# Performance work log

Hardware: AMD Instinct MI355X
Metric: run time of the kernel (lower is better)

## Reference

```python
import jax, jax.numpy as jnp
import numpy as np

N_NODES = 100000
N_EDGES = 3200000
NUM_TYPES = 8
TYPE_DIM = 16
IN_DIM = 5
HID = 64
HEADS = 2
OUT = 64
LN_EPS = 1e-5
NEG_SLOPE = 0.2


def segment_softmax(logits, seg, num_segments):
    # logits: [E, H], seg: [E] destination ids
    m = jax.ops.segment_max(logits, seg, num_segments=num_segments)
    m = jnp.where(jnp.isfinite(m), m, 0.0)
    e = jnp.exp(logits - m[seg])
    s = jax.ops.segment_sum(e, seg, num_segments=num_segments)
    return e / (s[seg] + 1e-16)


def gat_conv(x, W, a_src, a_dst, b, src, dst, n_nodes, heads, ch):
    # x: [N, F_in], W: [F_in, heads*ch], a_src/a_dst: [heads, ch], b: [heads*ch]
    h = (x @ W).reshape(n_nodes, heads, ch)            # [N, H, C]
    al_s = jnp.einsum('nhc,hc->nh', h, a_src)          # [N, H]
    al_d = jnp.einsum('nhc,hc->nh', h, a_dst)          # [N, H]
    e = jax.nn.leaky_relu(al_s[src] + al_d[dst], NEG_SLOPE)  # [E, H]
    alpha = segment_softmax(e, dst, n_nodes)           # [E, H]
    msg = alpha[:, :, None] * h[src]                   # [E, H, C]
    out = jax.ops.segment_sum(msg, dst, num_segments=n_nodes)  # [N, H, C]
    return out.reshape(n_nodes, heads * ch) + b


def setup_inputs() -> dict:
    key = jax.random.key(0)
    ks = jax.random.split(key, 16)
    in1 = IN_DIM + TYPE_DIM  # 21
    inp = {
        'x': jax.random.normal(ks[0], (N_NODES, IN_DIM), dtype=jnp.float32),
        'edge_index': jax.random.randint(ks[1], (2, N_EDGES), 0, N_NODES, dtype=jnp.int32),
        'type_ids': jax.random.randint(ks[2], (N_NODES,), 0, NUM_TYPES, dtype=jnp.int32),
        'type_emb': jax.random.normal(ks[3], (NUM_TYPES, TYPE_DIM), dtype=jnp.float32) * 0.3,
        'W1': jax.random.normal(ks[4], (in1, HID), dtype=jnp.float32) * (1.0 / np.sqrt(in1)),
        'a_src1': jax.random.normal(ks[5], (HEADS, HID // HEADS), dtype=jnp.float32) * 0.1,
        'a_dst1': jax.random.normal(ks[6], (HEADS, HID // HEADS), dtype=jnp.float32) * 0.1,
        'b1': jnp.zeros((HID,), dtype=jnp.float32),
        'W2': jax.random.normal(ks[7], (HID, OUT), dtype=jnp.float32) * (1.0 / np.sqrt(HID)),
        'a_src2': jax.random.normal(ks[8], (1, OUT), dtype=jnp.float32) * 0.1,
        'a_dst2': jax.random.normal(ks[9], (1, OUT), dtype=jnp.float32) * 0.1,
        'b2': jnp.zeros((OUT,), dtype=jnp.float32),
        'gamma': jnp.ones((OUT,), dtype=jnp.float32),
        'beta': jnp.zeros((OUT,), dtype=jnp.float32),
    }
    return inp


def reference(x, type_emb, W1, a_src1, a_dst1, b1, W2, a_src2, a_dst2, b2, gamma, beta, edge_index, type_ids):
    n = x.shape[0]
    # type embedding concat
    xin = jnp.concatenate([x, type_emb[type_ids]], axis=1)  # [N, 21]
    # add self loops (PyG GATConv default)
    loops = jnp.arange(n, dtype=edge_index.dtype)
    src = jnp.concatenate([edge_index[0], loops])
    dst = jnp.concatenate([edge_index[1], loops])
    h = gat_conv(xin, W1, a_src1, a_dst1, b1, src, dst, n, HEADS, HID // HEADS)
    h = jax.nn.relu(h)  # dropout = identity at inference
    h = gat_conv(h, W2, a_src2, a_dst2, b2, src, dst, n, 1, OUT)
    # LayerNorm
    mu = jnp.mean(h, axis=-1, keepdims=True)
    var = jnp.var(h, axis=-1, keepdims=True)
    return (h - mu) / jnp.sqrt(var + LN_EPS) * gamma + beta
```

## Files before the change

kernel.cpp:

```cpp
#include <hip/hip_runtime.h>
#include <hip/hip_fp16.h>

#define NEG_SLOPE 0.2f
#define BKT_SHIFT 8
#define BKT_NODES 256
#define BKT_CAP 10240
#define SRC_SHIFT 18
#define SRC_MASK 0x3FFFF
#define CHUNK 8192
#define NBMAX 512

typedef _Float16 half8 __attribute__((ext_vector_type(8)));
typedef float float4v __attribute__((ext_vector_type(4)));

__global__ void k_node1(const float* __restrict__ x, const int* __restrict__ type_ids,
                        const float* __restrict__ type_emb, const float* __restrict__ W1,
                        const float* __restrict__ a_src1, const float* __restrict__ a_dst1,
                        __half2* __restrict__ h1h, float* __restrict__ als1, float* __restrict__ ald1,
                        int N)
{
    int node = blockIdx.x * 4 + (threadIdx.x >> 6);
    int j = threadIdx.x & 63;
    if (node >= N) return;

    float xin[21];
#pragma unroll
    for (int k = 0; k < 5; k++) xin[k] = x[node * 5 + k];
    int t = type_ids[node];
#pragma unroll
    for (int k = 0; k < 16; k++) xin[5 + k] = type_emb[t * 16 + k];

    float h = 0.f;
#pragma unroll
    for (int k = 0; k < 21; k++) h += xin[k] * W1[k * 64 + j];

    float hn = __shfl_xor(h, 1);
    if ((j & 1) == 0)
        h1h[node * 32 + (j >> 1)] = __floats2half2_rn(h, hn);

    int head = j >> 5, lane = j & 31;
    float ps = h * a_src1[head * 32 + lane];
    float pd = h * a_dst1[head * 32 + lane];
#pragma unroll
    for (int m = 16; m >= 1; m >>= 1) { ps += __shfl_xor(ps, m); pd += __shfl_xor(pd, m); }
    if (lane == 0) { als1[node * 2 + head] = ps; ald1[node * 2 + head] = pd; }
}

__global__ __launch_bounds__(512) void k_bucketA(
        const int* __restrict__ ei, unsigned int* __restrict__ pk,
        int* __restrict__ bcnt, int E, int NBKT)
{
    __shared__ unsigned int stage[CHUNK];
    __shared__ unsigned short stageB[CHUNK];
    __shared__ int cnt[NBMAX];
    __shared__ int excl[NBMAX];
    __shared__ int curp[NBMAX];
    __shared__ int gbase[NBMAX];

    int t = threadIdx.x;
    int e0 = blockIdx.x * CHUNK;
    bool vec4 = ((E & 3) == 0);

    cnt[t] = 0;
    __syncthreads();

    int4 s4[4], d4[4];
    bool val[4];

    if (vec4) {
#pragma unroll
        for (int it = 0; it < 4; it++) {
            int e = e0 + it * 2048 + t * 4;
            val[it] = (e < E);
            if (val[it]) {
                s4[it] = *(const int4*)(ei + e);
                d4[it] = *(const int4*)(ei + (size_t)E + e);
                atomicAdd(&cnt[d4[it].x >> BKT_SHIFT], 1);
                atomicAdd(&cnt[d4[it].y >> BKT_SHIFT], 1);
                atomicAdd(&cnt[d4[it].z >> BKT_SHIFT], 1);
                atomicAdd(&cnt[d4[it].w >> BKT_SHIFT], 1);
            }
        }
    } else {
        for (int i = t; i < CHUNK; i += 512) {
            int e = e0 + i;
            if (e >= E) break;
            atomicAdd(&cnt[ei[E + e] >> BKT_SHIFT], 1);
        }
    }
    __syncthreads();
    int myc = cnt[t];
    __syncthreads();
    for (int off = 1; off < NBMAX; off <<= 1) {
        int v = (t >= off) ? cnt[t - off] : 0;
        __syncthreads();
        cnt[t] += v;
        __syncthreads();
    }
    {
        int ex = cnt[t] - myc;
        excl[t] = ex;
        curp[t] = ex;
        if (t < NBKT)
            gbase[t] = (myc > 0) ? atomicAdd(&bcnt[t], myc) : 0;
    }
    __syncthreads();
    if (vec4) {
#pragma unroll
        for (int it = 0; it < 4; it++) {
            if (!val[it]) continue;
            int ss[4] = {s4[it].x, s4[it].y, s4[it].z, s4[it].w};
            int dd[4] = {d4[it].x, d4[it].y, d4[it].z, d4[it].w};
#pragma unroll
            for (int k = 0; k < 4; k++) {
                int b = dd[k] >> BKT_SHIFT;
                int p = atomicAdd(&curp[b], 1);
                stage[p] = (unsigned)ss[k] | ((unsigned)(dd[k] & (BKT_NODES - 1)) << SRC_SHIFT);
                stageB[p] = (unsigned short)b;
            }
        }
    } else {
        for (int i = t; i < CHUNK; i += 512) {
            int e = e0 + i;
            if (e >= E) break;
            int s = ei[e], d = ei[E + e];
            int b = d >> BKT_SHIFT;
            int p = atomicAdd(&curp[b], 1);
            stage[p] = (unsigned)s | ((unsigned)(d & (BKT_NODES - 1)) << SRC_SHIFT);
            stageB[p] = (unsigned short)b;
        }
    }
    __syncthreads();
    int total = E - e0; if (total > CHUNK) total = CHUNK;
    for (int i = t; i < total; i += 512) {
        int b = stageB[i];
        int idx = gbase[b] + (i - excl[b]);
        if (idx < BKT_CAP) pk[(size_t)b * BKT_CAP + idx] = stage[i];
    }
}

__global__ __launch_bounds__(512) void k_build(
        const unsigned int* __restrict__ pk, const int* __restrict__ bcnt,
        int* __restrict__ rs, int* __restrict__ cur,
        int* __restrict__ ssrc, int N)
{
    __shared__ unsigned int vals[BKT_CAP];
    __shared__ int cnt[BKT_NODES];
    __shared__ int cursor[BKT_NODES];
    __shared__ int orig[BKT_NODES];
    __shared__ int red[512];
    int b = blockIdx.x;
    int t = threadIdx.x;
    int nb = min(bcnt[b], BKT_CAP);

    int part = 0;
    for (int i = t; i < b; i += 512) part += min(bcnt[i], BKT_CAP);
    red[t] = part;
    if (t < BKT_NODES) cnt[t] = 0;
    __syncthreads();
    for (int off = 256; off; off >>= 1) {
        if (t < off) red[t] += red[t + off];
        __syncthreads();
    }
    int bs = red[0];

    const unsigned int* mypk = pk + (size_t)b * BKT_CAP;
    int nb4 = nb & ~3;
    for (int e = t * 4; e < nb4; e += 2048) {
        uint4 v = *(const uint4*)(mypk + e);
        *(uint4*)(vals + e) = v;
        atomicAdd(&cnt[v.x >> SRC_SHIFT], 1);
        atomicAdd(&cnt[v.y >> SRC_SHIFT], 1);
        atomicAdd(&cnt[v.z >> SRC_SHIFT], 1);
        atomicAdd(&cnt[v.w >> SRC_SHIFT], 1);
    }
    for (int e = nb4 + t; e < nb; e += 512) {
        unsigned int v = mypk[e];
        vals[e] = v;
        atomicAdd(&cnt[v >> SRC_SHIFT], 1);
    }
    __syncthreads();
    if (t < BKT_NODES) orig[t] = cnt[t];
    __syncthreads();
    for (int off = 1; off < BKT_NODES; off <<= 1) {
        int v = (t < BKT_NODES && t >= off) ? cnt[t - off] : 0;
        __syncthreads();
        if (t < BKT_NODES) cnt[t] += v;
        __syncthreads();
    }
    if (t < BKT_NODES) {
        int c = orig[t];
        int ex = cnt[t] - c;
        cursor[t] = ex;
        int node = (b << BKT_SHIFT) + t;
        if (node < N) { rs[node] = bs + ex; cur[node] = bs + ex + c; }
    }
    __syncthreads();
    for (int e = t; e < nb; e += 512) {
        unsigned int w = vals[e];
        int p = atomicAdd(&cursor[w >> SRC_SHIFT], 1);
        ssrc[bs + p] = (int)(w & SRC_MASK);
    }
}

__global__ void k_gather1(const int* __restrict__ rs, const int* __restrict__ cur,
                          const int* __restrict__ ssrc, const float4* __restrict__ h4,
                          const float* __restrict__ als1, const float* __restrict__ ald1,
                          const float* __restrict__ b1, float4* __restrict__ h2h4, int N)
{
    int t = threadIdx.x;
    int l = t & 63;
    int q = l & 15;
    int i = q & 7;
    int hlf = q >> 3;
    int grpbase = l & 48;
    int head = i >> 2;

    int node = blockIdx.x * 16 + (t >> 4);
    bool live = node < N;
    int node_c = live ? node : (N - 1);

    int beg = rs[node_c];
    int cnt = live ? (cur[node_c] - beg) : 0;

    float ad0 = ald1[node_c * 2 + 0];
    float ad1 = ald1[node_c * 2 + 1];
    float ad = head ? ad1 : ad0;

    int mc = cnt;
    mc = max(mc, __shfl_xor(mc, 16));
    mc = max(mc, __shfl_xor(mc, 32));

    float acc[8];
#pragma unroll
    for (int k = 0; k < 8; k++) acc[k] = 0.f;
    float wsum = 0.f;

    for (int b = 0; b < mc; b += 16) {
        int slot = b + q;
        bool valid = slot < cnt;
        int idx = valid ? (beg + slot) : 0;
        int s = ssrc[idx];
        if (!valid) s = node_c;
        float2 al = *(const float2*)(als1 + (size_t)s * 2);
        float lg0 = al.x + ad0; lg0 = (lg0 >= 0.f) ? lg0 : NEG_SLOPE * lg0;
        float lg1 = al.y + ad1; lg1 = (lg1 >= 0.f) ? lg1 : NEG_SLOPE * lg1;
        float w0 = valid ? __expf(lg0) : 0.f;
        float w1 = valid ? __expf(lg1) : 0.f;
        __half2 wp = __floats2half2_rn(w0, w1);
        unsigned wpi = *(unsigned*)&wp;

#pragma unroll
        for (int r = 0; r < 8; r++) {
            int srcl = grpbase + hlf * 8 + r;
            int sr = __shfl(s, srcl);
            unsigned wri = __shfl(wpi, srcl);
            __half2 wh = *(__half2*)&wri;
            float w = head ? __high2float(wh) : __low2float(wh);
            float4 rv = h4[(size_t)sr * 8 + i];
            const __half* hp = (const __half*)&rv;
#pragma unroll
            for (int k = 0; k < 8; k++)
                acc[k] = fmaf(w, __half2float(hp[k]), acc[k]);
            wsum += w;
        }
    }

#pragma unroll
    for (int k = 0; k < 8; k++) acc[k] += __shfl_xor(acc[k], 8);
    wsum += __shfl_xor(wsum, 8);

    {
        float lg = als1[node_c * 2 + head] + ad;
        lg = (lg >= 0.f) ? lg : NEG_SLOPE * lg;
        float w = __expf(lg);
        float4 rv = h4[(size_t)node_c * 8 + i];
        const __half* hp = (const __half*)&rv;
#pragma unroll
        for (int k = 0; k < 8; k++)
            acc[k] = fmaf(w, __half2float(hp[k]), acc[k]);
        wsum += w;
    }

    float inv = 1.f / (wsum + 1e-16f);
    if (live && hlf == 0) {
        union { float4 f4; __half2 h2[4]; } u;
#pragma unroll
        for (int c = 0; c < 4; c++) {
            float v0 = fmaxf(acc[2*c]   * inv + b1[i * 8 + 2*c],     0.f);
            float v1 = fmaxf(acc[2*c+1] * inv + b1[i * 8 + 2*c + 1], 0.f);
            u.h2[c] = __floats2half2_rn(v0, v1);
        }
        h2h4[(size_t)node * 8 + i] = u.f4;
    }
}

__global__ __launch_bounds__(256) void k_node2m(
        const _Float16* __restrict__ h2h, const float* __restrict__ W2,
        const float* __restrict__ a_src2, const float* __restrict__ a_dst2,
        _Float16* __restrict__ h3h, float* __restrict__ als2, float* __restrict__ ald2, int N)
{
    __shared__ _Float16 w2t[64][72];
    __shared__ float h3t[4][16][65];
    int t = threadIdx.x;
    for (int e = t; e < 4096; e += 256) {
        int k = e >> 6, n = e & 63;
        w2t[n][k] = (_Float16)W2[e];
    }
    __syncthreads();

    int w = t >> 6, l = t & 63;
    int l15 = l & 15, quad = l >> 4;
    int nodebase = blockIdx.x * 64 + w * 16;

    int arow = nodebase + l15;
    if (arow >= N) arow = N - 1;
    const half8* ap = (const half8*)(h2h + (size_t)arow * 64 + quad * 8);
    half8 a0 = ap[0];
    half8 a1 = ap[4];
    float4v accs[4];
#pragma unroll
    for (int nt = 0; nt < 4; nt++) {
        half8 b0 = *(const half8*)(&w2t[nt * 16 + l15][quad * 8]);
        half8 b1 = *(const half8*)(&w2t[nt * 16 + l15][32 + quad * 8]);
        float4v c = {0.f, 0.f, 0.f, 0.f};
        c = __builtin_amdgcn_mfma_f32_16x16x32_f16(a0, b0, c, 0, 0, 0);
        c = __builtin_amdgcn_mfma_f32_16x16x32_f16(a1, b1, c, 0, 0, 0);
        accs[nt] = c;
    }
#pragma unroll
    for (int nt = 0; nt < 4; nt++)
#pragma unroll
        for (int r = 0; r < 4; r++)
            h3t[w][quad * 4 + r][nt * 16 + l15] = accs[nt][r];
    __syncthreads();

    int m = l >> 2, part = l & 3;
    int g = blockIdx.x * 64 + w * 16 + m;
    float ps = 0.f, pd = 0.f;
    union { float4 f4[2]; _Float16 h[16]; } u;
#pragma unroll
    for (int c = 0; c < 16; c++) {
        float v = h3t[w][m][part * 16 + c];
        ps += v * a_src2[part * 16 + c];
        pd += v * a_dst2[part * 16 + c];
        u.h[c] = (_Float16)v;
    }
    if (g < N) {
        float4* dst = (float4*)(h3h + (size_t)g * 64) + part * 2;
        dst[0] = u.f4[0];
        dst[1] = u.f4[1];
    }
    ps += __shfl_xor(ps, 1); ps += __shfl_xor(ps, 2);
    pd += __shfl_xor(pd, 1); pd += __shfl_xor(pd, 2);
    if (part == 0 && g < N) { als2[g] = ps; ald2[g] = pd; }
}

__global__ void k_gather2(const int* __restrict__ rs, const int* __restrict__ cur,
                          const int* __restrict__ ssrc, const float4* __restrict__ h4,
                          const float* __restrict__ als2, const float* __restrict__ ald2,
                          const float* __restrict__ b2, const float* __restrict__ gamma,
                          const float* __restrict__ beta, float* __restrict__ out, int N)
{
    int t = threadIdx.x;
    int l = t & 63;
    int q = l & 15;
    int i = q & 7;
    int hlf = q >> 3;
    int grpbase = l & 48;

    int node = blockIdx.x * 16 + (t >> 4);
    bool live = node < N;
    int node_c = live ? node : (N - 1);

    int beg = rs[node_c];
    int cnt = live ? (cur[node_c] - beg) : 0;
    float ad = ald2[node_c];

    int mc = cnt;
    mc = max(mc, __shfl_xor(mc, 16));
    mc = max(mc, __shfl_xor(mc, 32));

    float acc[8];
#pragma unroll
    for (int k = 0; k < 8; k++) acc[k] = 0.f;
    float wsum = 0.f;

    for (int b = 0; b < mc; b += 16) {
        int slot = b + q;
        bool valid = slot < cnt;
        int idx = valid ? (beg + slot) : 0;
        int s = ssrc[idx];
        if (!valid) s = node_c;
        float lg = als2[s] + ad;
        lg = (lg >= 0.f) ? lg : NEG_SLOPE * lg;
        float w = valid ? __expf(lg) : 0.f;

#pragma unroll
        for (int r = 0; r < 8; r++) {
            int srcl = grpbase + hlf * 8 + r;
            int sr = __shfl(s, srcl);
            float wr = __shfl(w, srcl);
            float4 rv = h4[(size_t)sr * 8 + i];
            const __half* hp = (const __half*)&rv;
#pragma unroll
            for (int k = 0; k < 8; k++)
                acc[k] = fmaf(wr, __half2float(hp[k]), acc[k]);
            wsum += wr;
        }
    }

#pragma unroll
    for (int k = 0; k < 8; k++) acc[k] += __shfl_xor(acc[k], 8);
    wsum += __shfl_xor(wsum, 8);

    {
        float lg = als2[node_c] + ad;
        lg = (lg >= 0.f) ? lg : NEG_SLOPE * lg;
        float w = __expf(lg);
        float4 rv = h4[(size_t)node_c * 8 + i];
        const __half* hp = (const __half*)&rv;
#pragma unroll
        for (int k = 0; k < 8; k++)
            acc[k] = fmaf(w, __half2float(hp[k]), acc[k]);
        wsum += w;
    }

    float inv = 1.f / (wsum + 1e-16f);
    float o[8];
    float s = 0.f;
#pragma unroll
    for (int k = 0; k < 8; k++) { o[k] = acc[k] * inv + b2[i * 8 + k]; s += o[k]; }
    s += __shfl_xor(s, 1); s += __shfl_xor(s, 2); s += __shfl_xor(s, 4);
    float mu = s * (1.f / 64.f);
    float v = 0.f;
#pragma unroll
    for (int k = 0; k < 8; k++) { float d = o[k] - mu; v += d * d; }
    v += __shfl_xor(v, 1); v += __shfl_xor(v, 2); v += __shfl_xor(v, 4);
    v *= (1.f / 64.f);
    float rstd = rsqrtf(v + 1e-5f);
    if (live && hlf == 0) {
        float res[8];
#pragma unroll
        for (int k = 0; k < 8; k++)
            res[k] = (o[k] - mu) * rstd * gamma[i * 8 + k] + beta[i * 8 + k];
        float4* op = (float4*)(out + (size_t)node * 64 + i * 8);
        op[0] = make_float4(res[0], res[1], res[2], res[3]);
        op[1] = make_float4(res[4], res[5], res[6], res[7]);
    }
}

extern "C" void kernel_launch(void* const* d_in, const int* in_sizes, int n_in,
                              void* d_out, int out_size, void* d_ws, size_t ws_size,
                              hipStream_t stream) {
    const float* x        = (const float*)d_in[0];
    const int*   ei       = (const int*)  d_in[1];
    const int*   type_ids = (const int*)  d_in[2];
    const float* type_emb = (const float*)d_in[3];
    const float* W1       = (const float*)d_in[4];
    const float* a_src1   = (const float*)d_in[5];
    const float* a_dst1   = (const float*)d_in[6];
    const float* b1       = (const float*)d_in[7];
    const float* W2       = (const float*)d_in[8];
    const float* a_src2   = (const float*)d_in[9];
    const float* a_dst2   = (const float*)d_in[10];
    const float* b2       = (const float*)d_in[11];
    const float* gamma    = (const float*)d_in[12];
    const float* beta     = (const float*)d_in[13];

    int N = in_sizes[0] / 5;
    int E = in_sizes[1] / 2;
    int NBKT = (N + BKT_NODES - 1) >> BKT_SHIFT;

    char* base = (char*)d_ws;
    size_t off = 0;
    auto carve = [&](size_t bytes) { void* p = base + off; off += (bytes + 255) & ~(size_t)255; return p; };
    __half2* h1h = (__half2*)carve((size_t)N * 64 * sizeof(__half));
    size_t pk_bytes = (size_t)NBKT * BKT_CAP * sizeof(unsigned int);
    size_t h23_bytes = 2 * (size_t)N * 64 * sizeof(__half);
    char* uni = (char*)carve(pk_bytes > h23_bytes ? pk_bytes : h23_bytes);
    _Float16* h2h = (_Float16*)uni;
    _Float16* h3h = (_Float16*)(uni + (size_t)N * 64 * sizeof(__half));
    unsigned int* pk = (unsigned int*)uni;
    float* als1  = (float*)carve((size_t)N * 2 * sizeof(float));
    float* ald1  = (float*)carve((size_t)N * 2 * sizeof(float));
    float* als2  = (float*)carve((size_t)N * sizeof(float));
    float* ald2  = (float*)carve((size_t)N * sizeof(float));
    int*   rs    = (int*)carve((size_t)N * sizeof(int));
    int*   cur   = (int*)carve((size_t)N * sizeof(int));
    int*   bcnt  = (int*)carve(1024 * sizeof(int));
    int*   ssrc  = (int*)carve((size_t)E * sizeof(int) + 256);

    dim3 tb(256);
    dim3 tb512(512);

    k_node1<<<dim3((N + 3) / 4), tb, 0, stream>>>(x, type_ids, type_emb, W1, a_src1, a_dst1,
                                                  h1h, als1, ald1, N);

    hipMemsetAsync(bcnt, 0, NBKT * sizeof(int), stream);
    k_bucketA<<<dim3((E + CHUNK - 1) / CHUNK), tb512, 0, stream>>>(ei, pk, bcnt, E, NBKT);
    k_build<<<dim3(NBKT), tb512, 0, stream>>>(pk, bcnt, rs, cur, ssrc, N);

    dim3 ng((N + 15) / 16);
    k_gather1<<<ng, tb, 0, stream>>>(rs, cur, ssrc, (const float4*)h1h, als1, ald1, b1,
                                     (float4*)h2h, N);
    k_node2m<<<dim3((N + 63) / 64), tb, 0, stream>>>(h2h, W2, a_src2, a_dst2,
                                                     h3h, als2, ald2, N);
    k_gather2<<<ng, tb, 0, stream>>>(rs, cur, ssrc, (const float4*)h3h, als2, ald2, b2,
                                     gamma, beta, (float*)d_out, N);
}
```

Measured before the change: 310.5 us.

## Use wave-shuffle scans and precompute bucket bases in separate kernel

Replaces the barrier-heavy Hillis-Steele shared-memory scans in the bucketing and CSR-build kernels with wavefront shuffle scans plus a small per-wave partial combine. A new single-block kernel computes the bucket base offsets once, so each build block no longer re-reduces all preceding bucket counts. The build kernel also drops its 40KB LDS staging of packed edges and re-reads them from global memory (likely L2), which should raise occupancy at the cost of a second global read. The extra kernel launch adds a small fixed overhead.

```diff
diff --git a/kernel.cpp b/kernel.cpp
--- a/kernel.cpp
+++ b/kernel.cpp
@@ -13,6 +13,15 @@
 typedef _Float16 half8 __attribute__((ext_vector_type(8)));
 typedef float float4v __attribute__((ext_vector_type(4)));
 
+__device__ __forceinline__ int wave_iscan(int v, int lane) {
+#pragma unroll
+    for (int off = 1; off < 64; off <<= 1) {
+        int u = __shfl_up(v, off);
+        if (lane >= off) v += u;
+    }
+    return v;
+}
+
 __global__ void k_node1(const float* __restrict__ x, const int* __restrict__ type_ids,
                         const float* __restrict__ type_emb, const float* __restrict__ W1,
                         const float* __restrict__ a_src1, const float* __restrict__ a_dst1,
@@ -56,8 +65,10 @@
     __shared__ int excl[NBMAX];
     __shared__ int curp[NBMAX];
     __shared__ int gbase[NBMAX];
+    __shared__ int wpart[8];
 
     int t = threadIdx.x;
+    int lane = t & 63, wv = t >> 6;
     int e0 = blockIdx.x * CHUNK;
     bool vec4 = ((E & 3) == 0);
 
@@ -90,15 +101,14 @@
     }
     __syncthreads();
     int myc = cnt[t];
-    __syncthreads();
-    for (int off = 1; off < NBMAX; off <<= 1) {
-        int v = (t >= off) ? cnt[t - off] : 0;
-        __syncthreads();
-        cnt[t] += v;
-        __syncthreads();
-    }
+    int incl = wave_iscan(myc, lane);
+    if (lane == 63) wpart[wv] = incl;
+    __syncthreads();
+#pragma unroll
+    for (int k = 0; k < 8; k++)
+        if (k < wv) incl += wpart[k];
     {
-        int ex = cnt[t] - myc;
+        int ex = incl - myc;
         excl[t] = ex;
         curp[t] = ex;
         if (t < NBKT)
@@ -139,65 +149,71 @@
     }
 }
 
+__global__ __launch_bounds__(512) void k_scanb(
+        const int* __restrict__ bcnt, int* __restrict__ bbase, int NBKT)
+{
+    __shared__ int wpart[8];
+    int t = threadIdx.x;
+    int lane = t & 63, wv = t >> 6;
+    int v = (t < NBKT) ? min(bcnt[t], BKT_CAP) : 0;
+    int incl = wave_iscan(v, lane);
+    if (lane == 63) wpart[wv] = incl;
+    __syncthreads();
+#pragma unroll
+    for (int k = 0; k < 8; k++)
+        if (k < wv) incl += wpart[k];
+    if (t < NBKT) bbase[t] = incl - v;
+}
+
 __global__ __launch_bounds__(512) void k_build(
         const unsigned int* __restrict__ pk, const int* __restrict__ bcnt,
+        const int* __restrict__ bbase,
         int* __restrict__ rs, int* __restrict__ cur,
         int* __restrict__ ssrc, int N)
 {
-    __shared__ unsigned int vals[BKT_CAP];
     __shared__ int cnt[BKT_NODES];
     __shared__ int cursor[BKT_NODES];
-    __shared__ int orig[BKT_NODES];
-    __shared__ int red[512];
+    __shared__ int wpart[4];
     int b = blockIdx.x;
     int t = threadIdx.x;
+    int lane = t & 63, wv = t >> 6;
     int nb = min(bcnt[b], BKT_CAP);
-
-    int part = 0;
-    for (int i = t; i < b; i += 512) part += min(bcnt[i], BKT_CAP);
-    red[t] = part;
+    int bs = bbase[b];
+
     if (t < BKT_NODES) cnt[t] = 0;
     __syncthreads();
-    for (int off = 256; off; off >>= 1) {
-        if (t < off) red[t] += red[t + off];
-        __syncthreads();
-    }
-    int bs = red[0];
 
     const unsigned int* mypk = pk + (size_t)b * BKT_CAP;
     int nb4 = nb & ~3;
     for (int e = t * 4; e < nb4; e += 2048) {
         uint4 v = *(const uint4*)(mypk + e);
-        *(uint4*)(vals + e) = v;
         atomicAdd(&cnt[v.x >> SRC_SHIFT], 1);
         atomicAdd(&cnt[v.y >> SRC_SHIFT], 1);
         atomicAdd(&cnt[v.z >> SRC_SHIFT], 1);
         atomicAdd(&cnt[v.w >> SRC_SHIFT], 1);
     }
     for (int e = nb4 + t; e < nb; e += 512) {
-        unsigned int v = mypk[e];
-        vals[e] = v;
-        atomicAdd(&cnt[v >> SRC_SHIFT], 1);
-    }
-    __syncthreads();
-    if (t < BKT_NODES) orig[t] = cnt[t];
-    __syncthreads();
-    for (int off = 1; off < BKT_NODES; off <<= 1) {
-        int v = (t < BKT_NODES && t >= off) ? cnt[t - off] : 0;
+        atomicAdd(&cnt[mypk[e] >> SRC_SHIFT], 1);
+    }
+    __syncthreads();
+    if (t < BKT_NODES) {
+        int myc = cnt[t];
+        int incl = wave_iscan(myc, lane);
+        if (lane == 63) wpart[wv] = incl;
         __syncthreads();
-        if (t < BKT_NODES) cnt[t] += v;
-        __syncthreads();
-    }
-    if (t < BKT_NODES) {
-        int c = orig[t];
-        int ex = cnt[t] - c;
+#pragma unroll
+        for (int k = 0; k < 4; k++)
+            if (k < wv) incl += wpart[k];
+        int ex = incl - myc;
         cursor[t] = ex;
         int node = (b << BKT_SHIFT) + t;
-        if (node < N) { rs[node] = bs + ex; cur[node] = bs + ex + c; }
+        if (node < N) { rs[node] = bs + ex; cur[node] = bs + ex + myc; }
+    } else {
+        __syncthreads();
     }
     __syncthreads();
     for (int e = t; e < nb; e += 512) {
-        unsigned int w = vals[e];
+        unsigned int w = mypk[e];
         int p = atomicAdd(&cursor[w >> SRC_SHIFT], 1);
         ssrc[bs + p] = (int)(w & SRC_MASK);
     }
@@ -489,6 +505,7 @@
     int*   rs    = (int*)carve((size_t)N * sizeof(int));
     int*   cur   = (int*)carve((size_t)N * sizeof(int));
     int*   bcnt  = (int*)carve(1024 * sizeof(int));
+    int*   bbase = (int*)carve(1024 * sizeof(int));
     int*   ssrc  = (int*)carve((size_t)E * sizeof(int) + 256);
 
     dim3 tb(256);
@@ -499,7 +516,8 @@
 
     hipMemsetAsync(bcnt, 0, NBKT * sizeof(int), stream);
     k_bucketA<<<dim3((E + CHUNK - 1) / CHUNK), tb512, 0, stream>>>(ei, pk, bcnt, E, NBKT);
-    k_build<<<dim3(NBKT), tb512, 0, stream>>>(pk, bcnt, rs, cur, ssrc, N);
+    k_scanb<<<dim3(1), tb512, 0, stream>>>(bcnt, bbase, NBKT);
+    k_build<<<dim3(NBKT), tb512, 0, stream>>>(pk, bcnt, bbase, rs, cur, ssrc, N);
 
     dim3 ng((N + 15) / 16);
     k_gather1<<<ng, tb, 0, stream>>>(rs, cur, ssrc, (const float4*)h1h, als1, ald1, b1,
```

New measurement: 308.9 us. About the same (-0.5%).
